# Performance work log

Measured on AMD Instinct MI355X. Metric: run time of the kernel, lower is better.

Reference implementation:

```python
import jax, jax.numpy as jnp
import numpy as np

B, L, D, H = 2, 2048, 512, 8
HD = D // H
DIL, WIN, CAUSAL = 2, 256, True
HIDDEN = 4 * D
EPS = 1e-5


def _layer_norm(x, w, b):
    m = jnp.mean(x, axis=-1, keepdims=True)
    v = jnp.mean(jnp.square(x - m), axis=-1, keepdims=True)
    return (x - m) * jax.lax.rsqrt(v + EPS) * w + b


def setup_inputs() -> dict:
    key = jax.random.key(0)
    ks = jax.random.split(key, 6)
    sc = 0.02
    return {
        "x": jax.random.normal(ks[0], (B, L, D), jnp.float32),
        "norm1_w": jnp.ones((D,), jnp.float32),
        "norm1_b": jnp.zeros((D,), jnp.float32),
        "qkv_w": jax.random.normal(ks[1], (3 * D, D), jnp.float32) * sc,
        "qkv_b": jnp.zeros((3 * D,), jnp.float32),
        "out_w": jax.random.normal(ks[2], (D, D), jnp.float32) * sc,
        "out_b": jnp.zeros((D,), jnp.float32),
        "norm2_w": jnp.ones((D,), jnp.float32),
        "norm2_b": jnp.zeros((D,), jnp.float32),
        "ffn_w1": jax.random.normal(ks[3], (HIDDEN, D), jnp.float32) * sc,
        "ffn_b1": jnp.zeros((HIDDEN,), jnp.float32),
        "ffn_w2": jax.random.normal(ks[4], (D, HIDDEN), jnp.float32) * sc,
        "ffn_b2": jnp.zeros((D,), jnp.float32),
    }


def reference(x, norm1_w, norm1_b, qkv_w, qkv_b, out_w, out_b,
              norm2_w, norm2_b, ffn_w1, ffn_b1, ffn_w2, ffn_b2):
    # pre-norm attention block
    h = _layer_norm(x, norm1_w, norm1_b)                       # [B,L,D]
    qkv = h @ qkv_w.T + qkv_b                                  # [B,L,3D]
    q, k, v = jnp.split(qkv, 3, axis=-1)

    def heads(t):  # [B,L,D] -> [B,H,L,HD]
        return t.reshape(B, L, H, HD).transpose(0, 2, 1, 3)

    q, k, v = heads(q), heads(k), heads(v)

    # dilated / windowed / causal keep mask (True = attend)
    idx = jnp.arange(L)
    delta = idx[:, None] - idx[None, :]                        # [L,L]
    keep = (delta % DIL) == 0
    keep &= jnp.abs(delta) <= WIN
    if CAUSAL:
        keep &= delta >= 0

    scale = 1.0 / np.sqrt(HD)
    scores = jnp.einsum('bhqd,bhkd->bhqk', q, k) * scale       # [B,H,L,L]
    scores = jnp.where(keep, scores, jnp.finfo(scores.dtype).min)
    attn = jax.nn.softmax(scores, axis=-1)
    o = jnp.einsum('bhqk,bhkd->bhqd', attn, v)                 # [B,H,L,HD]
    o = o.transpose(0, 2, 1, 3).reshape(B, L, D)
    o = o @ out_w.T + out_b

    x = x + o                                                  # residual (dropout p=0)

    # pre-norm FFN block
    h2 = _layer_norm(x, norm2_w, norm2_b)
    f = jax.nn.gelu(h2 @ ffn_w1.T + ffn_b1, approximate=False)
    f = f @ ffn_w2.T + ffn_b2
    return x + f
```

## Files before the change

### kernel.cpp

```cpp
#include <hip/hip_runtime.h>
#include <stdint.h>

typedef float f32x4 __attribute__((ext_vector_type(4)));
typedef unsigned short u16x4 __attribute__((ext_vector_type(4)));
typedef unsigned short u16x8 __attribute__((ext_vector_type(8)));
typedef __bf16 bf16x8 __attribute__((ext_vector_type(8)));

__device__ __forceinline__ unsigned short f2bf(float f) {
  unsigned u = __float_as_uint(f);
  u += 0x7fffu + ((u >> 16) & 1u);
  return (unsigned short)(u >> 16);
}
__device__ __forceinline__ float bf2f(unsigned short h) {
  return __uint_as_float(((unsigned)h) << 16);
}
__device__ __forceinline__ f32x4 mfma16x16x32(u16x8 a, u16x8 b, f32x4 c) {
  return __builtin_amdgcn_mfma_f32_16x16x32_bf16(
      __builtin_bit_cast(bf16x8, a), __builtin_bit_cast(bf16x8, b), c, 0, 0, 0);
}
__device__ __forceinline__ void gload_lds16(const unsigned short* g, unsigned short* l) {
  __builtin_amdgcn_global_load_lds((__attribute__((address_space(1))) void*)(g),
                                   (__attribute__((address_space(3))) void*)(l), 16, 0, 0);
}
__device__ __forceinline__ int xcd_swz(int bid, int nb) {
  int cpx = nb >> 3;
  return (bid & 7) * cpx + (bid >> 3);
}

__global__ __launch_bounds__(256)
void prep(const float* __restrict__ wq, const float* __restrict__ wo,
          const float* __restrict__ w1, const float* __restrict__ w2,
          unsigned short* __restrict__ dst,
          const float* __restrict__ x, const float* __restrict__ nw,
          const float* __restrict__ nb, unsigned short* __restrict__ hout) {
  if (blockIdx.x < 3072) {
    int i4 = blockIdx.x * 256 + threadIdx.x;
    int e = i4 << 2;
    const float* src; int off;
    if (e < 786432)       { src = wq; off = 0; }
    else if (e < 1048576) { src = wo; off = 786432; }
    else if (e < 2097152) { src = w1; off = 1048576; }
    else                  { src = w2; off = 2097152; }
    int le = e - off;
    f32x4 v = *(const f32x4*)(src + le);
    u16x4 o;
    #pragma unroll
    for (int i = 0; i < 4; ++i) o[i] = f2bf(v[i]);
    *(u16x4*)(dst + e) = o;
  } else {
    const int row = ((blockIdx.x - 3072) << 2) + (threadIdx.x >> 6);
    const int lane = threadIdx.x & 63;
    const float* xr = x + (size_t)row * 512 + (lane << 3);
    f32x4 v0 = *(const f32x4*)xr;
    f32x4 v1 = *(const f32x4*)(xr + 4);
    float s = 0.f, s2 = 0.f;
    #pragma unroll
    for (int i = 0; i < 4; ++i) { s += v0[i] + v1[i]; s2 += v0[i]*v0[i] + v1[i]*v1[i]; }
    #pragma unroll
    for (int m = 1; m < 64; m <<= 1) { s += __shfl_xor(s, m); s2 += __shfl_xor(s2, m); }
    float mean = s * (1.0f / 512.0f);
    float var  = s2 * (1.0f / 512.0f) - mean * mean;
    float rs = rsqrtf(var + 1e-5f);
    const int d = lane << 3;
    u16x8 o;
    #pragma unroll
    for (int i = 0; i < 8; ++i) {
      float xv = (i < 4) ? v0[i] : v1[i - 4];
      o[i] = f2bf((xv - mean) * rs * nw[d + i] + nb[d + i]);
    }
    *(u16x8*)(hout + (size_t)row * 512 + d) = o;
  }
}

__global__ __launch_bounds__(256)
void ln_bf16b(const unsigned short* __restrict__ x, const float* __restrict__ w,
              const float* __restrict__ b, unsigned short* __restrict__ out) {
  const int row = (blockIdx.x << 2) + (threadIdx.x >> 6);
  const int lane = threadIdx.x & 63;
  u16x8 xv = *(const u16x8*)(x + (size_t)row * 512 + (lane << 3));
  float f[8];
  float s = 0.f, s2 = 0.f;
  #pragma unroll
  for (int i = 0; i < 8; ++i) { f[i] = bf2f(xv[i]); s += f[i]; s2 += f[i]*f[i]; }
  #pragma unroll
  for (int m = 1; m < 64; m <<= 1) { s += __shfl_xor(s, m); s2 += __shfl_xor(s2, m); }
  float mean = s * (1.0f / 512.0f);
  float var  = s2 * (1.0f / 512.0f) - mean * mean;
  float rs = rsqrtf(var + 1e-5f);
  const int d = lane << 3;
  u16x8 o;
  #pragma unroll
  for (int i = 0; i < 8; ++i)
    o[i] = f2bf((f[i] - mean) * rs * w[d + i] + b[d + i]);
  *(u16x8*)(out + (size_t)row * 512 + d) = o;
}

template<int BM, int BN, int BK, int EPI, int WRV>
__global__ __launch_bounds__(256)
void gemm_bt(const unsigned short* __restrict__ A, const unsigned short* __restrict__ B,
             const float* __restrict__ bias, const float* __restrict__ residF,
             const unsigned short* __restrict__ residB,
             float* __restrict__ Cf, unsigned short* __restrict__ Cb,
             unsigned short* __restrict__ vt,
             int M, int N, int K) {
  constexpr int AM = BM / 32, AN = BN / 32;
  constexpr int CPR = BK / 8;
  constexpr int RPI = 2048 / BK;
  constexpr int LA = BM / RPI, LB = BN / RPI;
  constexpr int XM = (CPR - 1) < 7 ? (CPR - 1) : 7;
  __shared__ __align__(16) unsigned short lA[BM * BK];
  __shared__ __align__(16) unsigned short lB[BN * BK];
  const int tid = threadIdx.x;
  const int wave = tid >> 6, lane = tid & 63;
  const int bid = xcd_swz(blockIdx.x, gridDim.x);
  const int gn = N / BN;
  const int tm = bid / gn, tn = bid - tm * gn;
  const int m0 = tm * BM, n0 = tn * BN;
  const int wr = wave >> 1, wc = wave & 1;
  const int lr = lane & 15;
  const int lk = (lane >> 4) << 3;
  const int rit  = tid / CPR;
  const int csw  = ((tid % CPR) ^ (rit & XM)) << 3;
  f32x4 acc[AM][AN] = {};
  for (int k0 = 0; k0 < K; k0 += BK) {
    #pragma unroll
    for (int it = 0; it < LA; ++it)
      gload_lds16(A + (size_t)(m0 + it * RPI + rit) * K + k0 + csw,
                  &lA[((it << 8) + (wave << 6)) << 3]);
    #pragma unroll
    for (int it = 0; it < LB; ++it)
      gload_lds16(B + (size_t)(n0 + it * RPI + rit) * K + k0 + csw,
                  &lB[((it << 8) + (wave << 6)) << 3]);
    __syncthreads();
    #pragma unroll
    for (int kk = 0; kk < BK; kk += 32) {
      u16x8 af[AM], bfv[AN];
      #pragma unroll
      for (int m = 0; m < AM; ++m) {
        int row = wr * (BM / 2) + (m << 4) + lr;
        int sc = ((((kk + lk) >> 3) ^ (lr & XM)) << 3);
        af[m] = *(const u16x8*)&lA[row * BK + sc];
      }
      #pragma unroll
      for (int n = 0; n < AN; ++n) {
        int row = wc * (BN / 2) + (n << 4) + lr;
        int sc = ((((kk + lk) >> 3) ^ (lr & XM)) << 3);
        bfv[n] = *(const u16x8*)&lB[row * BK + sc];
      }
      #pragma unroll
      for (int m = 0; m < AM; ++m)
        #pragma unroll
        for (int n = 0; n < AN; ++n)
          acc[m][n] = mfma16x16x32(af[m], bfv[n], acc[m][n]);
    }
    __syncthreads();
  }
  const int rbase = m0 + wr * (BM / 2) + ((lane >> 4) << 2);
  const int cbase = n0 + wc * (BN / 2) + lr;
  #pragma unroll
  for (int m = 0; m < AM; ++m) {
    #pragma unroll
    for (int n = 0; n < AN; ++n) {
      int col = cbase + (n << 4);
      float bcol = bias[col];
      #pragma unroll
      for (int i = 0; i < 4; ++i) {
        int row = rbase + (m << 4) + i;
        float v = acc[m][n][i] + bcol;
        size_t off = (size_t)row * N + col;
        if (WRV && col >= 1024) {
          int hh = (col - 1024) >> 6, dd = (col - 1024) & 63;
          int bb = row >> 11, tok = row & 2047;
          long long vrow = ((((((long long)bb << 1) + (tok & 1)) << 3) + hh) << 6) + dd;
          vt[(vrow << 10) + (tok >> 1)] = f2bf(v);
        } else if (EPI == 0) {
          Cb[off] = f2bf(v);
        } else if (EPI == 2) {
          float g = 0.5f * v * (1.0f + erff(v * 0.70710678f));
          Cb[off] = f2bf(g);
        } else if (EPI == 3) {
          Cb[off] = f2bf(v + residF[off]);
        } else {
          Cf[off] = v + bf2f(residB[off]);
        }
      }
    }
  }
}

__global__ __launch_bounds__(256)
void attn_mfma(const unsigned short* __restrict__ qkv,
               const unsigned short* __restrict__ vt,
               unsigned short* __restrict__ out) {
  __shared__ __align__(16) unsigned short Pl[4][16 * 168];
  const int bid = xcd_swz(blockIdx.x, gridDim.x);
  const int qt  = bid & 15;
  const int par = (bid >> 4) & 1;
  const int h   = (bid >> 5) & 7;
  const int b   = bid >> 8;
  const int q0  = qt << 6;
  const int tid = threadIdx.x, wave = tid >> 6, lane = tid & 63;

  const int col = lane & 15;
  const int rg  = lane >> 4;
  const int qt0 = q0 + (wave << 4);
  unsigned short* Pw = Pl[wave];

  const long long qrow = (long long)((b << 11) + ((qt0 + col) << 1) + par);
  const unsigned short* qp = qkv + qrow * 1536 + (h << 6) + (rg << 3);
  u16x8 qa0 = *(const u16x8*)(qp);
  u16x8 qa1 = *(const u16x8*)(qp + 32);

  f32x4 sc[9];
  #pragma unroll
  for (int j = 0; j < 9; ++j) sc[j] = (f32x4){0.f, 0.f, 0.f, 0.f};
  #pragma unroll
  for (int j = 0; j < 9; ++j) {
    int kpj = qt0 - 128 + (j << 4) + col;
    long long krow = (long long)((b << 11) + (kpj << 1) + par);
    const unsigned short* kp = qkv + krow * 1536 + 512 + (h << 6) + (rg << 3);
    u16x8 k0 = *(const u16x8*)(kp);
    u16x8 k1 = *(const u16x8*)(kp + 32);
    sc[j] = mfma16x16x32(qa0, k0, sc[j]);
    sc[j] = mfma16x16x32(qa1, k1, sc[j]);
  }

  const long long vbase = ((long long)((((b << 1) + par) << 3) + h)) << 16;
  u16x8 vb[5][4];
  #pragma unroll
  for (int ks = 0; ks < 5; ++ks) {
    long long kp0 = (long long)qt0 - 128 + (ks << 5) + (rg << 3);
    #pragma unroll
    for (int n = 0; n < 4; ++n)
      vb[ks][n] = *(const u16x8*)(vt + vbase + (((long long)((n << 4) + col)) << 10) + kp0);
  }

  float mrow[4] = {-3e38f, -3e38f, -3e38f, -3e38f};
  #pragma unroll
  for (int j = 0; j < 9; ++j) {
    #pragma unroll
    for (int i = 0; i < 4; ++i) {
      int qr = (rg << 2) + i;
      int jk = (j << 4) + col;
      bool ok = (jk >= qr) && (jk <= qr + 128) && (qt0 + jk >= 128);
      float s = ok ? sc[j][i] * 0.125f : -1e30f;
      sc[j][i] = s;
      mrow[i] = fmaxf(mrow[i], s);
    }
  }
  #pragma unroll
  for (int i = 0; i < 4; ++i)
    #pragma unroll
    for (int m = 1; m < 16; m <<= 1) mrow[i] = fmaxf(mrow[i], __shfl_xor(mrow[i], m));

  float lrow[4] = {0.f, 0.f, 0.f, 0.f};
  #pragma unroll
  for (int j = 0; j < 9; ++j) {
    #pragma unroll
    for (int i = 0; i < 4; ++i) {
      float p = __expf(sc[j][i] - mrow[i]);
      lrow[i] += p;
      Pw[((rg << 2) + i) * 168 + (j << 4) + col] = f2bf(p);
    }
  }
  #pragma unroll
  for (int i = 0; i < 4; ++i)
    Pw[((rg << 2) + i) * 168 + 144 + col] = 0;
  #pragma unroll
  for (int i = 0; i < 4; ++i)
    #pragma unroll
    for (int m = 1; m < 16; m <<= 1) lrow[i] += __shfl_xor(lrow[i], m);
  float inv[4];
  #pragma unroll
  for (int i = 0; i < 4; ++i) inv[i] = 1.0f / lrow[i];

  f32x4 oacc[4] = {};
  #pragma unroll
  for (int ks = 0; ks < 5; ++ks) {
    u16x8 pa = *(const u16x8*)&Pw[col * 168 + (ks << 5) + (rg << 3)];
    #pragma unroll
    for (int n = 0; n < 4; ++n)
      oacc[n] = mfma16x16x32(pa, vb[ks][n], oacc[n]);
  }

  #pragma unroll
  for (int n = 0; n < 4; ++n) {
    #pragma unroll
    for (int i = 0; i < 4; ++i) {
      int q = qt0 + (rg << 2) + i;
      size_t off = ((size_t)((b << 11) + (q << 1) + par)) * 512 + (h << 6) + (n << 4) + col;
      out[off] = f2bf(oacc[n][i] * inv[i]);
    }
  }
}

extern "C" void kernel_launch(void* const* d_in, const int* in_sizes, int n_in,
                              void* d_out, int out_size, void* d_ws, size_t ws_size,
                              hipStream_t stream) {
  const float* x     = (const float*)d_in[0];
  const float* n1w   = (const float*)d_in[1];
  const float* n1b   = (const float*)d_in[2];
  const float* qkv_w = (const float*)d_in[3];
  const float* qkv_b = (const float*)d_in[4];
  const float* out_w = (const float*)d_in[5];
  const float* out_b = (const float*)d_in[6];
  const float* n2w   = (const float*)d_in[7];
  const float* n2b   = (const float*)d_in[8];
  const float* w1    = (const float*)d_in[9];
  const float* b1    = (const float*)d_in[10];
  const float* w2    = (const float*)d_in[11];
  const float* b2    = (const float*)d_in[12];

  char* ws = (char*)d_ws;
  unsigned short* wbf   = (unsigned short*)(ws);
  unsigned short* wq_bf = wbf;
  unsigned short* wo_bf = (unsigned short*)(ws + 1572864);
  unsigned short* w1_bf = (unsigned short*)(ws + 2097152);
  unsigned short* w2_bf = (unsigned short*)(ws + 4194304);
  unsigned short* h_bf  = (unsigned short*)(ws + 6291456);
  unsigned short* qkvb  = (unsigned short*)(ws + 10485760);
  unsigned short* ao_bf = (unsigned short*)(ws + 23068672);
  unsigned short* x1r   = (unsigned short*)(ws + 27262976);
  unsigned short* f1_bf = (unsigned short*)(ws + 10485760);
  unsigned short* vt    = (unsigned short*)(ws + 35651584);
  float* outp = (float*)d_out;

  prep<<<4096, 256, 0, stream>>>(qkv_w, out_w, w1, w2, wbf, x, n1w, n1b, h_bf);
  gemm_bt<128, 64, 128, 0, 1><<<32 * 24, 256, 0, stream>>>(
      h_bf, wq_bf, qkv_b, nullptr, nullptr, nullptr, qkvb, vt, 4096, 1536, 512);
  attn_mfma<<<512, 256, 0, stream>>>(qkvb, vt, ao_bf);
  gemm_bt<64, 64, 256, 3, 0><<<64 * 8, 256, 0, stream>>>(
      ao_bf, wo_bf, out_b, x, nullptr, nullptr, x1r, nullptr, 4096, 512, 512);
  ln_bf16b<<<1024, 256, 0, stream>>>(x1r, n2w, n2b, h_bf);
  gemm_bt<128, 128, 128, 2, 0><<<32 * 16, 256, 0, stream>>>(
      h_bf, w1_bf, b1, nullptr, nullptr, nullptr, f1_bf, nullptr, 4096, 2048, 512);
  gemm_bt<64, 64, 256, 4, 0><<<64 * 8, 256, 0, stream>>>(
      f1_bf, w2_bf, b2, nullptr, x1r, outp, nullptr, nullptr, 4096, 512, 2048);
}
```

Measured before the change: 84.49 us.

## Overlap weight conversion with attention, use tanh GELU and bf16 residual

Moves the bf16 conversion of out_w, ffn_w1 and ffn_w2 out of the prep kernel and into extra blocks appended to the attention launch. This shortens the critical path before the QKV GEMM and lets the conversion run alongside attention. The exact erf GELU is replaced with a tanh-style sigmoid approximation using __expf, and the residual x is now stored in bf16 by prep and read by the out-projection epilogue. Both numeric changes add approximation error: the GELU form and the bf16 rounding of the residual.

```diff
diff --git a/kernel.cpp b/kernel.cpp
--- a/kernel.cpp
+++ b/kernel.cpp
@@ -26,29 +26,26 @@
   int cpx = nb >> 3;
   return (bid & 7) * cpx + (bid >> 3);
 }
+__device__ __forceinline__ float gelu_f(float v) {
+  float z = 0.7978845608f * (v + 0.044715f * v * v * v);
+  float t = __expf(-2.0f * z);
+  return v * (1.0f / (1.0f + t));
+}
 
 __global__ __launch_bounds__(256)
-void prep(const float* __restrict__ wq, const float* __restrict__ wo,
-          const float* __restrict__ w1, const float* __restrict__ w2,
-          unsigned short* __restrict__ dst,
+void prep(const float* __restrict__ wq, unsigned short* __restrict__ dst,
           const float* __restrict__ x, const float* __restrict__ nw,
-          const float* __restrict__ nb, unsigned short* __restrict__ hout) {
-  if (blockIdx.x < 3072) {
-    int i4 = blockIdx.x * 256 + threadIdx.x;
-    int e = i4 << 2;
-    const float* src; int off;
-    if (e < 786432)       { src = wq; off = 0; }
-    else if (e < 1048576) { src = wo; off = 786432; }
-    else if (e < 2097152) { src = w1; off = 1048576; }
-    else                  { src = w2; off = 2097152; }
-    int le = e - off;
-    f32x4 v = *(const f32x4*)(src + le);
+          const float* __restrict__ nb, unsigned short* __restrict__ hout,
+          unsigned short* __restrict__ xbf) {
+  if (blockIdx.x < 768) {
+    int e = (blockIdx.x * 256 + threadIdx.x) << 2;
+    f32x4 v = *(const f32x4*)(wq + e);
     u16x4 o;
     #pragma unroll
     for (int i = 0; i < 4; ++i) o[i] = f2bf(v[i]);
     *(u16x4*)(dst + e) = o;
   } else {
-    const int row = ((blockIdx.x - 3072) << 2) + (threadIdx.x >> 6);
+    const int row = ((blockIdx.x - 768) << 2) + (threadIdx.x >> 6);
     const int lane = threadIdx.x & 63;
     const float* xr = x + (size_t)row * 512 + (lane << 3);
     f32x4 v0 = *(const f32x4*)xr;
@@ -62,13 +59,15 @@
     float var  = s2 * (1.0f / 512.0f) - mean * mean;
     float rs = rsqrtf(var + 1e-5f);
     const int d = lane << 3;
-    u16x8 o;
+    u16x8 o, xo;
     #pragma unroll
     for (int i = 0; i < 8; ++i) {
       float xv = (i < 4) ? v0[i] : v1[i - 4];
+      xo[i] = f2bf(xv);
       o[i] = f2bf((xv - mean) * rs * nw[d + i] + nb[d + i]);
     }
     *(u16x8*)(hout + (size_t)row * 512 + d) = o;
+    *(u16x8*)(xbf  + (size_t)row * 512 + d) = xo;
   }
 }
 
@@ -98,7 +97,7 @@
 template<int BM, int BN, int BK, int EPI, int WRV>
 __global__ __launch_bounds__(256)
 void gemm_bt(const unsigned short* __restrict__ A, const unsigned short* __restrict__ B,
-             const float* __restrict__ bias, const float* __restrict__ residF,
+             const float* __restrict__ bias,
              const unsigned short* __restrict__ residB,
              float* __restrict__ Cf, unsigned short* __restrict__ Cb,
              unsigned short* __restrict__ vt,
@@ -176,10 +175,9 @@
         } else if (EPI == 0) {
           Cb[off] = f2bf(v);
         } else if (EPI == 2) {
-          float g = 0.5f * v * (1.0f + erff(v * 0.70710678f));
-          Cb[off] = f2bf(g);
-        } else if (EPI == 3) {
-          Cb[off] = f2bf(v + residF[off]);
+          Cb[off] = f2bf(gelu_f(v));
+        } else if (EPI == 5) {
+          Cb[off] = f2bf(v + bf2f(residB[off]));
         } else {
           Cf[off] = v + bf2f(residB[off]);
         }
@@ -191,9 +189,24 @@
 __global__ __launch_bounds__(256)
 void attn_mfma(const unsigned short* __restrict__ qkv,
                const unsigned short* __restrict__ vt,
-               unsigned short* __restrict__ out) {
+               unsigned short* __restrict__ out,
+               const float* __restrict__ wo, const float* __restrict__ w1,
+               const float* __restrict__ w2, unsigned short* __restrict__ wdst) {
+  if (blockIdx.x >= 512) {
+    int e = ((blockIdx.x - 512) * 256 + threadIdx.x) << 2;
+    const float* src; int off;
+    if (e < 262144)        { src = wo; off = 0; }
+    else if (e < 1310720)  { src = w1; off = 262144; }
+    else                   { src = w2; off = 1310720; }
+    f32x4 v = *(const f32x4*)(src + e - off);
+    u16x4 o;
+    #pragma unroll
+    for (int i = 0; i < 4; ++i) o[i] = f2bf(v[i]);
+    *(u16x4*)(wdst + 786432 + e) = o;
+    return;
+  }
   __shared__ __align__(16) unsigned short Pl[4][16 * 168];
-  const int bid = xcd_swz(blockIdx.x, gridDim.x);
+  const int bid = xcd_swz(blockIdx.x, 512);
   const int qt  = bid & 15;
   const int par = (bid >> 4) & 1;
   const int h   = (bid >> 5) & 7;
@@ -323,17 +336,18 @@
   unsigned short* x1r   = (unsigned short*)(ws + 27262976);
   unsigned short* f1_bf = (unsigned short*)(ws + 10485760);
   unsigned short* vt    = (unsigned short*)(ws + 35651584);
+  unsigned short* xbf   = (unsigned short*)(ws + 44040192);
   float* outp = (float*)d_out;
 
-  prep<<<4096, 256, 0, stream>>>(qkv_w, out_w, w1, w2, wbf, x, n1w, n1b, h_bf);
+  prep<<<1792, 256, 0, stream>>>(qkv_w, wbf, x, n1w, n1b, h_bf, xbf);
   gemm_bt<128, 64, 128, 0, 1><<<32 * 24, 256, 0, stream>>>(
-      h_bf, wq_bf, qkv_b, nullptr, nullptr, nullptr, qkvb, vt, 4096, 1536, 512);
-  attn_mfma<<<512, 256, 0, stream>>>(qkvb, vt, ao_bf);
-  gemm_bt<64, 64, 256, 3, 0><<<64 * 8, 256, 0, stream>>>(
-      ao_bf, wo_bf, out_b, x, nullptr, nullptr, x1r, nullptr, 4096, 512, 512);
+      h_bf, wq_bf, qkv_b, nullptr, nullptr, qkvb, vt, 4096, 1536, 512);
+  attn_mfma<<<512 + 2304, 256, 0, stream>>>(qkvb, vt, ao_bf, out_w, w1, w2, wbf);
+  gemm_bt<64, 64, 256, 5, 0><<<64 * 8, 256, 0, stream>>>(
+      ao_bf, wo_bf, out_b, xbf, nullptr, x1r, nullptr, 4096, 512, 512);
   ln_bf16b<<<1024, 256, 0, stream>>>(x1r, n2w, n2b, h_bf);
   gemm_bt<128, 128, 128, 2, 0><<<32 * 16, 256, 0, stream>>>(
-      h_bf, w1_bf, b1, nullptr, nullptr, nullptr, f1_bf, nullptr, 4096, 2048, 512);
+      h_bf, w1_bf, b1, nullptr, nullptr, f1_bf, nullptr, 4096, 2048, 512);
   gemm_bt<64, 64, 256, 4, 0><<<64 * 8, 256, 0, stream>>>(
-      f1_bf, w2_bf, b2, nullptr, x1r, outp, nullptr, nullptr, 4096, 512, 2048);
-}
+      f1_bf, w2_bf, b2, x1r, outp, nullptr, nullptr, 4096, 512, 2048);
+}
```

New measurement: 84.00 us, median of 2. About the same (-0.6%).
